# Performance work log

Hardware: AMD Instinct MI355X
Metric: run time of the kernel (lower is better)

## Reference

```python
import jax, jax.numpy as jnp
import numpy as np

N_HEAD = 16
LN_EPS = 1e-5     # torch LayerNorm default
ATTN_EPS = 1e-6   # fast-transformers CausalLinearAttention eps


def layer_norm(x, g, b):
    mu = x.mean(-1, keepdims=True)
    var = ((x - mu) ** 2).mean(-1, keepdims=True)
    return (x - mu) * jax.lax.rsqrt(var + LN_EPS) * g + b


def favor(x, omega):
    # Favor/Performer softmax-kernel features.
    # x: [B,S,H,dh], omega: [dh, m/2] -> phi: [B,S,H,m] with m = 2*(dh//2) = dh
    dh = x.shape[-1]
    m = 2 * omega.shape[-1]
    xs = x * (dh ** -0.25)  # x * sqrt(softmax_temp), softmax_temp = 1/sqrt(dh)
    u = jnp.einsum('bshd,dm->bshm', xs, omega)
    h = 0.5 * jnp.sum(xs * xs, axis=-1, keepdims=True)  # ||x||^2 / 2
    return jnp.concatenate([jnp.exp(u - h), jnp.exp(-u - h)], axis=-1) * (m ** -0.5)


def causal_linear_attention(q, k, v):
    # q,k: [B,S,H,M] feature-mapped; v: [B,S,H,Dv]
    # out[i] = (phiQ_i @ sum_{j<=i} phiK_j v_j^T) / (phiQ_i . sum_{j<=i} phiK_j)
    B, S, H, M = q.shape
    Dv = v.shape[-1]
    qT = jnp.moveaxis(q, 1, 0)  # [S,B,H,M]
    kT = jnp.moveaxis(k, 1, 0)
    vT = jnp.moveaxis(v, 1, 0)  # [S,B,H,Dv]
    S0 = jnp.zeros((B, H, M, Dv), q.dtype)
    z0 = jnp.zeros((B, H, M), q.dtype)

    def step(carry, qkv):
        Sst, zst = carry
        qi, ki, vi = qkv
        Sst = Sst + ki[..., :, None] * vi[..., None, :]  # [B,H,M,Dv]
        zst = zst + ki                                   # [B,H,M]
        num = jnp.einsum('bhm,bhmd->bhd', qi, Sst)
        den = jnp.einsum('bhm,bhm->bh', qi, zst) + ATTN_EPS
        return (Sst, zst), num / den[..., None]

    _, out = jax.lax.scan(step, (S0, z0), (qT, kT, vT))
    return jnp.moveaxis(out, 0, 1)  # [B,S,H,Dv]


def forward(x, Wq, bq, Wk, bk, Wv, bv, Wo, bo, omega,
            ln1_g, ln1_b, ln2_g, ln2_b, W1, bf1, W2, bf2):
    L = Wq.shape[0]
    B, S, D = x.shape
    dh = D // N_HEAD
    out = x
    for l in range(L):  # fixed small layer count
        q = (out @ Wq[l] + bq[l]).reshape(B, S, N_HEAD, dh)
        k = (out @ Wk[l] + bk[l]).reshape(B, S, N_HEAD, dh)
        v = (out @ Wv[l] + bv[l]).reshape(B, S, N_HEAD, dh)
        Qf = favor(q, omega[l])
        Kf = favor(k, omega[l])
        a = causal_linear_attention(Qf, Kf, v).reshape(B, S, D)
        a = a @ Wo[l] + bo[l]
        h = layer_norm(out + a, ln1_g[l], ln1_b[l])          # norm1 (post-norm)
        y = jax.nn.relu(h @ W1[l] + bf1[l]) @ W2[l] + bf2[l]  # FFN
        out = layer_norm(h + y, ln2_g[l], ln2_b[l])          # norm2
    return out


def setup_inputs() -> dict:
    key = jax.random.key(0)
    L, B, S, D, DFF = 3, 2, 1024, 1024, 4096
    dh = D // N_HEAD
    ks = jax.random.split(key, 8)
    g = lambda k, shape: jax.random.normal(k, shape, jnp.float32) * 0.02
    return {
        'x': jax.random.normal(ks[0], (B, S, D), jnp.float32),
        'Wq': g(ks[1], (L, D, D)), 'bq': jnp.zeros((L, D), jnp.float32),
        'Wk': g(ks[2], (L, D, D)), 'bk': jnp.zeros((L, D), jnp.float32),
        'Wv': g(ks[3], (L, D, D)), 'bv': jnp.zeros((L, D), jnp.float32),
        'Wo': g(ks[4], (L, D, D)), 'bo': jnp.zeros((L, D), jnp.float32),
        'omega': jax.random.normal(ks[5], (L, dh, dh // 2), jnp.float32),
        'ln1_g': jnp.ones((L, D), jnp.float32), 'ln1_b': jnp.zeros((L, D), jnp.float32),
        'ln2_g': jnp.ones((L, D), jnp.float32), 'ln2_b': jnp.zeros((L, D), jnp.float32),
        'W1': g(ks[6], (L, D, DFF)), 'bf1': jnp.zeros((L, DFF), jnp.float32),
        'W2': g(ks[7], (L, DFF, D)), 'bf2': jnp.zeros((L, D), jnp.float32),
    }


def reference(x, Wq, bq, Wk, bk, Wv, bv, Wo, bo, omega,
              ln1_g, ln1_b, ln2_g, ln2_b, W1, bf1, W2, bf2):
    return forward(x, Wq, bq, Wk, bk, Wv, bv, Wo, bo, omega,
                   ln1_g, ln1_b, ln2_g, ln2_b, W1, bf1, W2, bf2)
```

## Files before the change

kernel.cpp:

```cpp
#include <hip/hip_runtime.h>

typedef unsigned int u32;
typedef unsigned short u16;
typedef unsigned long long u64;

#define LN_EPS 1e-5f
#define ATTN_EPS 1e-6f

typedef __bf16 bf16x8 __attribute__((ext_vector_type(8)));
typedef short shortx8 __attribute__((ext_vector_type(8)));
typedef float fx4 __attribute__((ext_vector_type(4)));
typedef float fx16 __attribute__((ext_vector_type(16)));

__device__ __forceinline__ u16 f2bf(float f){
  union{float f; u32 u;} x; x.f = f;
  u32 r = 0x7fffu + ((x.u>>16)&1u);
  return (u16)((x.u + r)>>16);
}
__device__ __forceinline__ float bf2f(u16 u){
  union{u32 u; float f;} x; x.u = ((u32)u)<<16; return x.f;
}
__device__ __forceinline__ bf16x8 ldfrag(const u16* p){
  return __builtin_bit_cast(bf16x8, *(const shortx8*)p);
}

__device__ __forceinline__ void async16(const void* g, void* l){
  typedef const __attribute__((address_space(1))) void gas_t;
  typedef __attribute__((address_space(3))) void las_t;
  __builtin_amdgcn_global_load_lds((gas_t*)(u64)g, (las_t*)(u32)(u64)l, 16, 0, 0);
}

__global__ void detect_kernel(const u16* __restrict__ ln1g, int* __restrict__ flag){
  if (threadIdx.x == 0 && blockIdx.x == 0)
    *flag = (ln1g[0] == 0x3F80u) ? 1 : 0;
}

__global__ __launch_bounds__(256) void cvt_small(
    const void* p0, const void* p1, const void* p2, const void* p3,
    const void* p4, const void* p5, const void* p6, const void* p7,
    const void* p8, const void* p9, const void* p10,
    float* __restrict__ out, const int* __restrict__ flagp)
{
  int i = blockIdx.x*256 + threadIdx.x;
  if (i >= 46080) return;
  const void* src; int off;
  if      (i < 3072)  { src=p0;  off=i; }
  else if (i < 6144)  { src=p1;  off=i-3072; }
  else if (i < 9216)  { src=p2;  off=i-6144; }
  else if (i < 12288) { src=p3;  off=i-9216; }
  else if (i < 18432) { src=p4;  off=i-12288; }
  else if (i < 21504) { src=p5;  off=i-18432; }
  else if (i < 24576) { src=p6;  off=i-21504; }
  else if (i < 27648) { src=p7;  off=i-24576; }
  else if (i < 30720) { src=p8;  off=i-27648; }
  else if (i < 43008) { src=p9;  off=i-30720; }
  else                { src=p10; off=i-43008; }
  float v;
  if (*flagp){ union{u32 u; float f;} x; x.u = ((u32)((const u16*)src)[off])<<16; v = x.f; }
  else v = ((const float*)src)[off];
  out[i] = v;
}

__global__ __launch_bounds__(256) void cvt_x(const void* __restrict__ in, float* __restrict__ out,
                                             u16* __restrict__ outbf, int n, const int* __restrict__ flagp){
  int i = blockIdx.x*256 + threadIdx.x;
  if (i >= n) return;
  float v;
  if (*flagp){ union{u32 u; float f;} x; x.u = ((u32)((const u16*)in)[i])<<16; v = x.f; }
  else v = ((const float*)in)[i];
  out[i] = v;
  outbf[i] = f2bf(v);
}

__global__ __launch_bounds__(256) void transpose_cvtL(
    const void* __restrict__ W, u16* __restrict__ Wt,
    int K, int N, size_t zsrc, size_t zdst, const int* __restrict__ flagp)
{
  __shared__ float s[32][33];
  const size_t eoff = (size_t)blockIdx.z * zsrc;
  Wt += (size_t)blockIdx.z * zdst;
  const int bx = blockIdx.x, by = blockIdx.y;
  const int tid = threadIdx.x;
  const int c = tid & 31, r = tid >> 5;
  const int isbf = *flagp;
#pragma unroll
  for (int i = 0; i < 4; ++i){
    int k = by*32 + r + i*8, n = bx*32 + c;
    size_t idx = eoff + (size_t)k*N + n;
    float v;
    if (isbf){ union{u32 u; float f;} x; x.u = ((u32)((const u16*)W)[idx])<<16; v = x.f; }
    else v = ((const float*)W)[idx];
    s[r + i*8][c] = v;
  }
  __syncthreads();
#pragma unroll
  for (int i = 0; i < 4; ++i){
    int n = bx*32 + r + i*8, k = by*32 + c;
    Wt[(size_t)n*K + k] = f2bf(s[c][r + i*8]);
  }
}

__global__ __launch_bounds__(256) void transpose_cvtQ(
    const void* __restrict__ W0, const void* __restrict__ W1,
    const void* __restrict__ W2, const void* __restrict__ W3,
    u16* __restrict__ Wt, const int* __restrict__ flagp)
{
  __shared__ float s[32][33];
  const int z = blockIdx.z, l = z >> 2, m = z & 3;
  const void* W = (m==0)?W0:((m==1)?W1:((m==2)?W2:W3));
  const size_t eoff = (size_t)l * 1048576;
  Wt += (size_t)z * 1048576;
  const int bx = blockIdx.x, by = blockIdx.y;
  const int tid = threadIdx.x;
  const int c = tid & 31, r = tid >> 5;
  const int isbf = *flagp;
#pragma unroll
  for (int i = 0; i < 4; ++i){
    int k = by*32 + r + i*8, n = bx*32 + c;
    size_t idx = eoff + (size_t)k*1024 + n;
    float v;
    if (isbf){ union{u32 u; float f;} x; x.u = ((u32)((const u16*)W)[idx])<<16; v = x.f; }
    else v = ((const float*)W)[idx];
    s[r + i*8][c] = v;
  }
  __syncthreads();
#pragma unroll
  for (int i = 0; i < 4; ++i){
    int n = bx*32 + r + i*8, k = by*32 + c;
    Wt[(size_t)n*1024 + k] = f2bf(s[c][r + i*8]);
  }
}

__global__ __launch_bounds__(256, 2) void mfma_gemm(
    const u16* __restrict__ A, const u16* __restrict__ W,
    const float* __restrict__ bias,
    float* __restrict__ C, u16* __restrict__ Cbf,
    int N, int Kst, int kstep_z, int klen,
    size_t wz, size_t cz, int bz, int bias_all, int relu)
{
  __shared__ u16 As[2][128*64];
  __shared__ u16 Bs[2][128*64];
  const int z = blockIdx.z;
  W    += (size_t)z * wz;
  bias += (size_t)z * bz;
  if (C) C += (size_t)z * cz;
  const int kbeg = z * kstep_z;
  const int tid = threadIdx.x;
  const int lane = tid & 63, wid = tid >> 6;

  int bx = blockIdx.x, by = blockIdx.y;
  {
    const int gx = gridDim.x, gy = gridDim.y;
    if (((gx & 3) == 0) && ((gy & 1) == 0)) {
      const int cw = gx >> 2, ch = gy >> 1;
      if (((cw & (cw-1)) == 0) && ((ch & (ch-1)) == 0)) {
        const int o = by*gx + bx;
        const int xcd = o & 7, k = o >> 3;
        const int lgw = 31 - __clz(cw);
        bx = (xcd & 3)*cw + (k & (cw-1));
        by = (xcd >> 2)*ch + (k >> lgw);
      }
    }
  }
  const int row0 = by * 128, col0 = bx * 128;

  const int sR = tid >> 3;
  const int sC = ((tid & 7) ^ (sR & 7)) << 3;
  const u16* gA = A + (size_t)(row0 + sR)*Kst + kbeg + sC;
  const u16* gB = W + (size_t)(col0 + sR)*Kst + kbeg + sC;
  const int lb = tid*8;

  const int iters = klen >> 6;
#pragma unroll
  for (int i = 0; i < 4; ++i){
    async16(gA + (size_t)(32*i)*Kst, &As[0][i*2048 + lb]);
    async16(gB + (size_t)(32*i)*Kst, &Bs[0][i*2048 + lb]);
  }
  __builtin_amdgcn_s_waitcnt(0x0F70);
  __builtin_amdgcn_s_barrier();

  const int l31 = lane & 31, hi = lane >> 5;
  const int wr = (wid >> 1) * 64, wc = (wid & 1) * 64;
  fx16 acc[2][2] = {};

  for (int t = 0; t < iters; ++t){
    const int cur = t & 1;
    if (t + 1 < iters){
      const int ko = (t + 1) << 6;
#pragma unroll
      for (int i = 0; i < 4; ++i){
        async16(gA + (size_t)(32*i)*Kst + ko, &As[cur^1][i*2048 + lb]);
        async16(gB + (size_t)(32*i)*Kst + ko, &Bs[cur^1][i*2048 + lb]);
      }
    }
    bf16x8 af0[4], af1[4], bg0[4], bg1[4];
#pragma unroll
    for (int kh = 0; kh < 4; ++kh){
      const int sl = (((2*kh + hi) ^ (l31 & 7))) << 3;
      af0[kh] = ldfrag(&As[cur][(wr      + l31)*64 + sl]);
      af1[kh] = ldfrag(&As[cur][(wr + 32 + l31)*64 + sl]);
      bg0[kh] = ldfrag(&Bs[cur][(wc      + l31)*64 + sl]);
      bg1[kh] = ldfrag(&Bs[cur][(wc + 32 + l31)*64 + sl]);
    }
    __builtin_amdgcn_s_setprio(1);
#pragma unroll
    for (int kh = 0; kh < 4; ++kh){
      acc[0][0] = __builtin_amdgcn_mfma_f32_32x32x16_bf16(af0[kh], bg0[kh], acc[0][0], 0,0,0);
      acc[0][1] = __builtin_amdgcn_mfma_f32_32x32x16_bf16(af0[kh], bg1[kh], acc[0][1], 0,0,0);
      acc[1][0] = __builtin_amdgcn_mfma_f32_32x32x16_bf16(af1[kh], bg0[kh], acc[1][0], 0,0,0);
      acc[1][1] = __builtin_amdgcn_mfma_f32_32x32x16_bf16(af1[kh], bg1[kh], acc[1][1], 0,0,0);
    }
    __builtin_amdgcn_s_setprio(0);
    __builtin_amdgcn_s_waitcnt(0x0F70);
    __builtin_amdgcn_s_barrier();
  }

  const int rbase = 4*hi;
#pragma unroll
  for (int nt = 0; nt < 2; ++nt){
    const int col = col0 + wc + nt*32 + l31;
    const float bv = (bias_all || z == 0) ? bias[col] : 0.f;
#pragma unroll
    for (int mt = 0; mt < 2; ++mt){
#pragma unroll
      for (int r = 0; r < 16; ++r){
        const int row = row0 + wr + mt*32 + rbase + (r & 3) + 8*(r >> 2);
        float v = acc[mt][nt][r] + bv;
        if (relu) v = fmaxf(v, 0.f);
        if (C)   C[(size_t)row*N + col] = v;
        if (Cbf) Cbf[(size_t)row*N + col] = f2bf(v);
      }
    }
  }
}

__global__ __launch_bounds__(256) void favor_kernel(
    float* __restrict__ Q, float* __restrict__ Kp, const float* __restrict__ omega,
    u16* __restrict__ Qb, u16* __restrict__ Kb)
{
  __shared__ float sh[4][64];
  __shared__ float sho[64][32];
  int tid = threadIdx.x;
  for (int i = tid; i < 2048; i += 256)
    sho[i>>5][i&31] = omega[i];
  int wv = tid >> 6, lane = tid & 63;
  int th = blockIdx.x*4 + wv;
  size_t base = (size_t)(th >> 4) * 1024 + (size_t)(th & 15) * 64;
  int jm = lane & 31;
  float sgn = (lane < 32) ? 1.f : -1.f;
  for (int w = 0; w < 2; ++w){
    float* p = w ? Kp : Q;
    float xs = p[base + lane] * 0.35355339059327373f;
    __syncthreads();
    sh[wv][lane] = xs;
    __syncthreads();
    float u = 0.f, hh = 0.f;
#pragma unroll
    for (int d = 0; d < 64; ++d){
      float xv = sh[wv][d];
      u  = fmaf(xv, sho[d][jm], u);
      hh = fmaf(xv, xv, hh);
    }
    float phi = expf(sgn*u - 0.5f*hh) * 0.125f;
    if (w) p[base + lane] = phi;
    (w ? Kb : Qb)[base + lane] = f2bf(phi);
  }
}

__global__ __launch_bounds__(256) void chunk_kv(
    const float* __restrict__ Kf, const float* __restrict__ V,
    float* __restrict__ KV, float* __restrict__ Ksum)
{
  __shared__ float Ks[64][64];
  __shared__ float Vs[64][64];
  int blk = blockIdx.x;
  int c = blk & 15, h = (blk >> 4) & 15, b = blk >> 8;
  int tid = threadIdx.x;
  for (int i = tid; i < 1024; i += 256){
    int j = i >> 4, m4 = (i & 15) << 2;
    size_t src = ((size_t)(b*1024 + c*64 + j)*16 + h)*64 + m4;
    *(float4*)&Ks[j][m4] = *(const float4*)&Kf[src];
    *(float4*)&Vs[j][m4] = *(const float4*)&V[src];
  }
  __syncthreads();
  int m = tid & 63, dg = tid >> 6;
  float acc[16] = {0.f};
  for (int j = 0; j < 64; ++j){
    float kv = Ks[j][m];
#pragma unroll
    for (int di = 0; di < 16; ++di)
      acc[di] = fmaf(Vs[j][dg*16+di], kv, acc[di]);
  }
  size_t outb = (size_t)blk * 4096;
#pragma unroll
  for (int di = 0; di < 16; ++di)
    KV[outb + (size_t)(dg*16+di)*64 + m] = acc[di];
  if (tid < 64){
    float s = 0.f;
    for (int j = 0; j < 64; ++j) s += Ks[j][tid];
    Ksum[(size_t)blk*64 + tid] = s;
  }
}

__global__ __launch_bounds__(256) void chunk_scan(float* __restrict__ KV, float* __restrict__ Ksum)
{
  int blk = blockIdx.x;
  int bh = blk >> 4, ec = blk & 15;
  int e = ec*256 + threadIdx.x;
  size_t base = (size_t)bh * 65536 + e;
  float run = 0.f;
  for (int c = 0; c < 16; ++c){
    size_t idx = base + (size_t)c*4096;
    float t = KV[idx]; KV[idx] = run; run += t;
  }
  if (ec == 0 && threadIdx.x < 64){
    size_t kb = (size_t)bh * 1024 + threadIdx.x;
    float rz = 0.f;
    for (int c = 0; c < 16; ++c){
      size_t idx = kb + c*64;
      float t = Ksum[idx]; Ksum[idx] = rz; rz += t;
    }
  }
}

__global__ __launch_bounds__(256) void attn_kernel(
    const u16* __restrict__ Qbf, const u16* __restrict__ Kbf,
    const float* __restrict__ V, const float* __restrict__ KVt,
    const float* __restrict__ Ksum, u16* __restrict__ Outbf)
{
  __shared__ u16 Qs[64][72];
  __shared__ u16 Ks[64][72];
  __shared__ u16 Ss[64][72];
  __shared__ u16 Vt[64][72];
  __shared__ u16 Pt[64][72];
  __shared__ float Vrow[64][68];
  __shared__ float densum[64];

  const int blk = blockIdx.x;
  const int c = blk & 15, h = (blk >> 4) & 15, b = blk >> 8;
  const int tid = threadIdx.x;
  const int lane = tid & 63, w = tid >> 6;
  const int quad = lane >> 4, l16 = lane & 15;
  const int t0 = b*1024 + c*64;

  {
    const int r = tid >> 2, q4 = (tid & 3) << 4;
    size_t g = (size_t)(t0 + r)*1024 + h*64 + q4;
    *(uint4*)&Qs[r][q4]   = *(const uint4*)(Qbf + g);
    *(uint4*)&Qs[r][q4+8] = *(const uint4*)(Qbf + g + 8);
    *(uint4*)&Ks[r][q4]   = *(const uint4*)(Kbf + g);
    *(uint4*)&Ks[r][q4+8] = *(const uint4*)(Kbf + g + 8);
    const float* vg = V + g;
    *(float4*)&Vrow[r][q4+0]  = *(const float4*)(vg+0);
    *(float4*)&Vrow[r][q4+4]  = *(const float4*)(vg+4);
    *(float4*)&Vrow[r][q4+8]  = *(const float4*)(vg+8);
    *(float4*)&Vrow[r][q4+12] = *(const float4*)(vg+12);
    const float* pg = KVt + (size_t)blk*4096 + r*64 + q4;
    u16 tmp[16];
#pragma unroll
    for (int j = 0; j < 16; ++j) tmp[j] = f2bf(pg[j]);
    *(uint4*)&Pt[r][q4]   = *(uint4*)&tmp[0];
    *(uint4*)&Pt[r][q4+8] = *(uint4*)&tmp[8];
  }
  __syncthreads();
  {
    const int d = tid >> 2, j16 = (tid & 3) << 4;
    u16 tmp[16];
#pragma unroll
    for (int j = 0; j < 16; ++j) tmp[j] = f2bf(Vrow[j16+j][d]);
    *(uint4*)&Vt[d][j16]   = *(uint4*)&tmp[0];
    *(uint4*)&Vt[d][j16+8] = *(uint4*)&tmp[8];
  }

  const int iw0 = w*16;
  bf16x8 aq0 = ldfrag(&Qs[iw0+l16][quad*8]);
  bf16x8 aq1 = ldfrag(&Qs[iw0+l16][32+quad*8]);
  fx4 sacc[4];
#pragma unroll
  for (int u = 0; u < 4; ++u){
    sacc[u] = (fx4){0.f,0.f,0.f,0.f};
    bf16x8 b0 = ldfrag(&Ks[u*16+l16][quad*8]);
    bf16x8 b1 = ldfrag(&Ks[u*16+l16][32+quad*8]);
    sacc[u] = __builtin_amdgcn_mfma_f32_16x16x32_bf16(aq0, b0, sacc[u], 0, 0, 0);
    sacc[u] = __builtin_amdgcn_mfma_f32_16x16x32_bf16(aq1, b1, sacc[u], 0, 0, 0);
  }
  float rs[4] = {0.f,0.f,0.f,0.f};
#pragma unroll
  for (int u = 0; u < 4; ++u){
    const int jl = u*16 + l16;
#pragma unroll
    for (int r = 0; r < 4; ++r){
      const int il = iw0 + quad*4 + r;
      float v = (jl <= il) ? sacc[u][r] : 0.f;
      rs[r] += v;
      Ss[il][jl] = f2bf(v);
    }
  }
#pragma unroll
  for (int off = 1; off < 16; off <<= 1){
#pragma unroll
    for (int r = 0; r < 4; ++r) rs[r] += __shfl_xor(rs[r], off);
  }
  if (l16 == 0){
#pragma unroll
    for (int r = 0; r < 4; ++r) densum[iw0 + quad*4 + r] = rs[r];
  }
  __syncthreads();

  {
    const int row = iw0 + l16;
    const float* zp = Ksum + (size_t)blk*64;
    float dp = 0.f;
#pragma unroll
    for (int m = 0; m < 16; ++m){
      const int mm = quad*16 + m;
      dp = fmaf(bf2f(Qs[row][mm]), zp[mm], dp);
    }
    dp += __shfl_xor(dp, 16);
    dp += __shfl_xor(dp, 32);
    if (quad == 0) densum[row] = densum[row] + dp + ATTN_EPS;
  }
  __syncthreads();

  bf16x8 as0 = ldfrag(&Ss[iw0+l16][quad*8]);
  bf16x8 as1 = ldfrag(&Ss[iw0+l16][32+quad*8]);
  fx4 oacc[4];
#pragma unroll
  for (int u = 0; u < 4; ++u){
    const int d0 = u*16;
    oacc[u] = (fx4){0.f,0.f,0.f,0.f};
    oacc[u] = __builtin_amdgcn_mfma_f32_16x16x32_bf16(as0, ldfrag(&Vt[d0+l16][quad*8]),    oacc[u], 0,0,0);
    oacc[u] = __builtin_amdgcn_mfma_f32_16x16x32_bf16(as1, ldfrag(&Vt[d0+l16][32+quad*8]), oacc[u], 0,0,0);
    oacc[u] = __builtin_amdgcn_mfma_f32_16x16x32_bf16(aq0, ldfrag(&Pt[d0+l16][quad*8]),    oacc[u], 0,0,0);
    oacc[u] = __builtin_amdgcn_mfma_f32_16x16x32_bf16(aq1, ldfrag(&Pt[d0+l16][32+quad*8]), oacc[u], 0,0,0);
  }
#pragma unroll
  for (int u = 0; u < 4; ++u){
    const int d = u*16 + l16;
#pragma unroll
    for (int r = 0; r < 4; ++r){
      const int il = iw0 + quad*4 + r;
      const float o = oacc[u][r] / densum[il];
      Outbf[(size_t)(t0 + il)*1024 + h*64 + d] = f2bf(o);
    }
  }
}

__global__ __launch_bounds__(256) void resid_ln(
    const float* __restrict__ X, const float* __restrict__ Y0, const float* __restrict__ Y1,
    const float* __restrict__ Y2, const float* __restrict__ Y3,
    const float* __restrict__ g, const float* __restrict__ b,
    float* __restrict__ Dst, u16* __restrict__ DstBf,
    void* __restrict__ OutPtr, const int* __restrict__ flagp)
{
  __shared__ float rs[4], rss[4];
  int row = blockIdx.x, tid = threadIdx.x;
  int lane = tid & 63, wv = tid >> 6;
  size_t base = (size_t)row * 1024;
  int c = tid << 2;
  float4 xv = *(const float4*)&X[base + c];
  float4 y0 = *(const float4*)&Y0[base + c];
  float4 y1 = *(const float4*)&Y1[base + c];
  float v0 = xv.x+y0.x+y1.x, v1 = xv.y+y0.y+y1.y, v2 = xv.z+y0.z+y1.z, v3 = xv.w+y0.w+y1.w;
  if (Y2){
    float4 y2 = *(const float4*)&Y2[base + c];
    float4 y3 = *(const float4*)&Y3[base + c];
    v0 += y2.x + y3.x; v1 += y2.y + y3.y; v2 += y2.z + y3.z; v3 += y2.w + y3.w;
  }
  float s = v0+v1+v2+v3;
  float ss = v0*v0+v1*v1+v2*v2+v3*v3;
  for (int off = 32; off; off >>= 1){
    s  += __shfl_down(s, off);
    ss += __shfl_down(ss, off);
  }
  if (lane == 0){ rs[wv] = s; rss[wv] = ss; }
  __syncthreads();
  float S  = rs[0]+rs[1]+rs[2]+rs[3];
  float SS = rss[0]+rss[1]+rss[2]+rss[3];
  float mu = S * (1.f/1024.f);
  float var = SS * (1.f/1024.f) - mu*mu;
  float rinv = rsqrtf(var + LN_EPS);
  float4 gv = *(const float4*)(g + c);
  float4 bb = *(const float4*)(b + c);
  float o0 = (v0-mu)*rinv*gv.x + bb.x;
  float o1 = (v1-mu)*rinv*gv.y + bb.y;
  float o2 = (v2-mu)*rinv*gv.z + bb.z;
  float o3 = (v3-mu)*rinv*gv.w + bb.w;
  *(float4*)&Dst[base + c] = make_float4(o0,o1,o2,o3);
  uint2 ob;
  ob.x = (u32)f2bf(o0) | ((u32)f2bf(o1) << 16);
  ob.y = (u32)f2bf(o2) | ((u32)f2bf(o3) << 16);
  *(uint2*)(DstBf + base + c) = ob;
  if (OutPtr){
    if (*flagp){
      *(uint2*)((u16*)OutPtr + base + c) = ob;
    } else {
      *(float4*)((float*)OutPtr + base + c) = make_float4(o0,o1,o2,o3);
    }
  }
}

extern "C" void kernel_launch(void* const* d_in, const int* in_sizes, int n_in,
                              void* d_out, int out_size, void* d_ws, size_t ws_size,
                              hipStream_t stream)
{
  (void)in_sizes; (void)n_in; (void)out_size; (void)ws_size;

  float* ws   = (float*)d_ws;
  float* R    = ws;
  float* P0   = R  + 2097152;
  float* P1   = P0 + 2097152;
  float* P2   = P1 + 2097152;
  float* P3   = P2 + 2097152;
  float* KVb  = P3 + 2097152;
  float* Ks   = KVb + 2097152;
  float* smallP = Ks + 32768;
  float* pend = smallP + 46080;
  int* flag = (int*)pend;
  u16* abf  = (u16*)(pend + 4);
  u16* hbf  = abf  + 2097152;
  u16* t1bf = hbf  + 2097152;
  u16* fbf  = t1bf + 2097152;
  u16* qpbf = fbf  + 8388608;
  u16* kpbf = qpbf + 2097152;
  u16* WtQ  = kpbf + 2097152;
  u16* WtF1 = WtQ  + 12582912;
  u16* WtF2 = WtF1 + 12582912;

  float* bqF  = smallP + 0;
  float* boF  = smallP + 9216;
  float* omF  = smallP + 12288;
  float* l1gF = smallP + 18432;
  float* l1bF = smallP + 21504;
  float* l2gF = smallP + 24576;
  float* l2bF = smallP + 27648;
  float* bf1F = smallP + 30720;
  float* bf2F = smallP + 43008;

  detect_kernel<<<1, 64, 0, stream>>>((const u16*)d_in[10], flag);
  cvt_small<<<180, 256, 0, stream>>>(d_in[2], d_in[4], d_in[6], d_in[8], d_in[9],
                                     d_in[10], d_in[11], d_in[12], d_in[13],
                                     d_in[15], d_in[17], smallP, flag);
  cvt_x<<<8192, 256, 0, stream>>>(d_in[0], R, abf, 2097152, flag);

  transpose_cvtQ<<<dim3(32, 32, 12), 256, 0, stream>>>(d_in[1], d_in[3], d_in[5], d_in[7],
                                                       WtQ, flag);
  transpose_cvtL<<<dim3(128, 32, 3), 256, 0, stream>>>(d_in[14], WtF1, 1024, 4096,
                                                       4194304, 4194304, flag);
  transpose_cvtL<<<dim3(32, 128, 3), 256, 0, stream>>>(d_in[16], WtF2, 4096, 1024,
                                                       4194304, 4194304, flag);

  dim3 gQKV(8, 16, 3);
  dim3 gO(8, 16, 2);
  dim3 gF1(32, 16, 1);
  dim3 gF2(8, 16, 4);

  for (int l = 0; l < 3; ++l){
    const size_t wQ = (size_t)l * 4194304;

    mfma_gemm<<<gQKV, 256, 0, stream>>>(abf, WtQ + wQ, bqF + l*1024, P0, (u16*)nullptr,
                                        1024, 1024, 0, 1024,
                                        1048576, 2097152, 3072, 1, 0);
    favor_kernel<<<8192, 256, 0, stream>>>(P0, P1, omF + l*2048, qpbf, kpbf);
    chunk_kv<<<512, 256, 0, stream>>>(P1, P2, KVb, Ks);
    chunk_scan<<<512, 256, 0, stream>>>(KVb, Ks);
    attn_kernel<<<512, 256, 0, stream>>>(qpbf, kpbf, P2, KVb, Ks, t1bf);

    mfma_gemm<<<gO, 256, 0, stream>>>(t1bf, WtQ + wQ + 3145728, boF + l*1024, P0, (u16*)nullptr,
                                      1024, 1024, 512, 512,
                                      0, 2097152, 0, 0, 0);
    resid_ln<<<2048, 256, 0, stream>>>(R, P0, P1, nullptr, nullptr,
                                       l1gF + l*1024, l1bF + l*1024,
                                       KVb, hbf, nullptr, flag);

    mfma_gemm<<<gF1, 256, 0, stream>>>(hbf, WtF1 + wQ, bf1F + l*4096, (float*)nullptr, fbf,
                                       4096, 1024, 0, 1024,
                                       0, 0, 0, 1, 1);

    mfma_gemm<<<gF2, 256, 0, stream>>>(fbf, WtF2 + wQ, bf2F + l*1024, P0, (u16*)nullptr,
                                       1024, 4096, 1024, 1024,
                                       0, 2097152, 0, 0, 0);

    resid_ln<<<2048, 256, 0, stream>>>(KVb, P0, P1, P2, P3,
                                       l2gF + l*1024, l2bF + l*1024,
                                       R, abf, (l == 2) ? d_out : nullptr, flag);
  }
}
```

Baseline: 727.5 us.

## Switch GEMM to 256x128 tiles with 8 waves and triple-buffered split staging

The bf16 MFMA GEMM now uses 512-thread blocks computing 256x128 output tiles, with three LDS buffers and a prefetch distance of two k-steps. Each k-step's global-to-LDS copy is split into two halves interleaved with the two halves of the MFMA work. The goal is to hide global-load latency and reuse the B tile across more rows. In exchange the grids halve in the M dimension: the QKV and O-projection launches drop to 192 and 128 blocks, which can leave CUs idle. The 144KB of LDS limits occupancy to one block per CU.

```diff
diff --git a/kernel.cpp b/kernel.cpp
--- a/kernel.cpp
+++ b/kernel.cpp
@@ -131,15 +131,15 @@
   }
 }
 
-__global__ __launch_bounds__(256, 2) void mfma_gemm(
+__global__ __launch_bounds__(512, 2) void mfma_gemm8(
     const u16* __restrict__ A, const u16* __restrict__ W,
     const float* __restrict__ bias,
     float* __restrict__ C, u16* __restrict__ Cbf,
     int N, int Kst, int kstep_z, int klen,
     size_t wz, size_t cz, int bz, int bias_all, int relu)
 {
-  __shared__ u16 As[2][128*64];
-  __shared__ u16 Bs[2][128*64];
+  __shared__ u16 As[3][256*64];
+  __shared__ u16 Bs[3][128*64];
   const int z = blockIdx.z;
   W    += (size_t)z * wz;
   bias += (size_t)z * bz;
@@ -147,6 +147,7 @@
   const int kbeg = z * kstep_z;
   const int tid = threadIdx.x;
   const int lane = tid & 63, wid = tid >> 6;
+  const size_t KstS = (size_t)Kst;
 
   int bx = blockIdx.x, by = blockIdx.y;
   {
@@ -162,76 +163,108 @@
       }
     }
   }
-  const int row0 = by * 128, col0 = bx * 128;
+  const int row0 = by * 256, col0 = bx * 128;
 
   const int sR = tid >> 3;
   const int sC = ((tid & 7) ^ (sR & 7)) << 3;
-  const u16* gA = A + (size_t)(row0 + sR)*Kst + kbeg + sC;
-  const u16* gB = W + (size_t)(col0 + sR)*Kst + kbeg + sC;
-  const int lb = tid*8;
-
-  const int iters = klen >> 6;
-#pragma unroll
-  for (int i = 0; i < 4; ++i){
-    async16(gA + (size_t)(32*i)*Kst, &As[0][i*2048 + lb]);
-    async16(gB + (size_t)(32*i)*Kst, &Bs[0][i*2048 + lb]);
+  const u16* gAr = A + (size_t)(row0 + sR)*KstS + kbeg + sC;
+  const u16* gBr = W + (size_t)(col0 + sR)*KstS + kbeg + sC;
+
+#define STAGE_H0(b, ks) { const size_t ko = (size_t)(ks) << 6; \
+    async16(gAr + ko,                &As[b][tid*8]); \
+    async16(gAr + 64*KstS + ko,      &As[b][4096 + tid*8]); \
+    async16(gBr + ko,                &Bs[b][tid*8]); }
+#define STAGE_H1(b, ks) { const size_t ko = (size_t)(ks) << 6; \
+    async16(gAr + 128*KstS + ko,     &As[b][8192 + tid*8]); \
+    async16(gAr + 192*KstS + ko,     &As[b][12288 + tid*8]); \
+    async16(gBr + 64*KstS + ko,      &Bs[b][4096 + tid*8]); }
+
+  const int nt = klen >> 6;
+  STAGE_H0(0, 0) STAGE_H1(0, 0)
+  STAGE_H0(1, 1) STAGE_H1(1, 1)
+  __builtin_amdgcn_s_waitcnt(0x0F76);
+  __builtin_amdgcn_s_barrier();
+
+  const int l31 = lane & 31, hi = lane >> 5;
+  const int wr = (wid >> 1) * 64;
+  const int wc = (wid & 1) * 64;
+  fx16 acc[2][2] = {};
+
+  for (int t = 0; t < nt; ++t){
+    const int buf = t % 3;
+    const int nx   = (t + 2 < nt) ? (t + 2) : (nt - 1);
+    const int nbuf = (t + 2) % 3;
+
+    bf16x8 a0[2][2], b0[2][2];
+#pragma unroll
+    for (int kk = 0; kk < 2; ++kk){
+      const int sl = ((2*kk + hi) ^ (l31 & 7)) << 3;
+#pragma unroll
+      for (int mt = 0; mt < 2; ++mt)
+        a0[mt][kk] = ldfrag(&As[buf][(wr + mt*32 + l31)*64 + sl]);
+#pragma unroll
+      for (int ntc = 0; ntc < 2; ++ntc)
+        b0[ntc][kk] = ldfrag(&Bs[buf][(wc + ntc*32 + l31)*64 + sl]);
+    }
+    STAGE_H0(nbuf, nx)
+    __builtin_amdgcn_s_barrier();
+    __builtin_amdgcn_s_setprio(1);
+#pragma unroll
+    for (int kk = 0; kk < 2; ++kk)
+#pragma unroll
+      for (int mt = 0; mt < 2; ++mt)
+#pragma unroll
+        for (int ntc = 0; ntc < 2; ++ntc)
+          acc[mt][ntc] = __builtin_amdgcn_mfma_f32_32x32x16_bf16(a0[mt][kk], b0[ntc][kk], acc[mt][ntc], 0,0,0);
+    __builtin_amdgcn_s_setprio(0);
+    __builtin_amdgcn_s_barrier();
+
+    bf16x8 a1[2][2], b1[2][2];
+#pragma unroll
+    for (int kk = 0; kk < 2; ++kk){
+      const int sl = ((2*(kk+2) + hi) ^ (l31 & 7)) << 3;
+#pragma unroll
+      for (int mt = 0; mt < 2; ++mt)
+        a1[mt][kk] = ldfrag(&As[buf][(wr + mt*32 + l31)*64 + sl]);
+#pragma unroll
+      for (int ntc = 0; ntc < 2; ++ntc)
+        b1[ntc][kk] = ldfrag(&Bs[buf][(wc + ntc*32 + l31)*64 + sl]);
+    }
+    STAGE_H1(nbuf, nx)
+    __builtin_amdgcn_s_waitcnt(0x0F76);
+    __builtin_amdgcn_s_barrier();
+    __builtin_amdgcn_s_setprio(1);
+#pragma unroll
+    for (int kk = 0; kk < 2; ++kk)
+#pragma unroll
+      for (int mt = 0; mt < 2; ++mt)
+#pragma unroll
+        for (int ntc = 0; ntc < 2; ++ntc)
+          acc[mt][ntc] = __builtin_amdgcn_mfma_f32_32x32x16_bf16(a1[mt][kk], b1[ntc][kk], acc[mt][ntc], 0,0,0);
+    __builtin_amdgcn_s_setprio(0);
+    __builtin_amdgcn_s_barrier();
   }
   __builtin_amdgcn_s_waitcnt(0x0F70);
-  __builtin_amdgcn_s_barrier();
-
-  const int l31 = lane & 31, hi = lane >> 5;
-  const int wr = (wid >> 1) * 64, wc = (wid & 1) * 64;
-  fx16 acc[2][2] = {};
-
-  for (int t = 0; t < iters; ++t){
-    const int cur = t & 1;
-    if (t + 1 < iters){
-      const int ko = (t + 1) << 6;
-#pragma unroll
-      for (int i = 0; i < 4; ++i){
-        async16(gA + (size_t)(32*i)*Kst + ko, &As[cur^1][i*2048 + lb]);
-        async16(gB + (size_t)(32*i)*Kst + ko, &Bs[cur^1][i*2048 + lb]);
-      }
-    }
-    bf16x8 af0[4], af1[4], bg0[4], bg1[4];
-#pragma unroll
-    for (int kh = 0; kh < 4; ++kh){
-      const int sl = (((2*kh + hi) ^ (l31 & 7))) << 3;
-      af0[kh] = ldfrag(&As[cur][(wr      + l31)*64 + sl]);
-      af1[kh] = ldfrag(&As[cur][(wr + 32 + l31)*64 + sl]);
-      bg0[kh] = ldfrag(&Bs[cur][(wc      + l31)*64 + sl]);
-      bg1[kh] = ldfrag(&Bs[cur][(wc + 32 + l31)*64 + sl]);
-    }
-    __builtin_amdgcn_s_setprio(1);
-#pragma unroll
-    for (int kh = 0; kh < 4; ++kh){
-      acc[0][0] = __builtin_amdgcn_mfma_f32_32x32x16_bf16(af0[kh], bg0[kh], acc[0][0], 0,0,0);
-      acc[0][1] = __builtin_amdgcn_mfma_f32_32x32x16_bf16(af0[kh], bg1[kh], acc[0][1], 0,0,0);
-      acc[1][0] = __builtin_amdgcn_mfma_f32_32x32x16_bf16(af1[kh], bg0[kh], acc[1][0], 0,0,0);
-      acc[1][1] = __builtin_amdgcn_mfma_f32_32x32x16_bf16(af1[kh], bg1[kh], acc[1][1], 0,0,0);
-    }
-    __builtin_amdgcn_s_setprio(0);
-    __builtin_amdgcn_s_waitcnt(0x0F70);
-    __builtin_amdgcn_s_barrier();
-  }
 
   const int rbase = 4*hi;
 #pragma unroll
-  for (int nt = 0; nt < 2; ++nt){
-    const int col = col0 + wc + nt*32 + l31;
+  for (int ntc = 0; ntc < 2; ++ntc){
+    const int col = col0 + wc + ntc*32 + l31;
     const float bv = (bias_all || z == 0) ? bias[col] : 0.f;
 #pragma unroll
     for (int mt = 0; mt < 2; ++mt){
 #pragma unroll
       for (int r = 0; r < 16; ++r){
         const int row = row0 + wr + mt*32 + rbase + (r & 3) + 8*(r >> 2);
-        float v = acc[mt][nt][r] + bv;
+        float v = acc[mt][ntc][r] + bv;
         if (relu) v = fmaxf(v, 0.f);
         if (C)   C[(size_t)row*N + col] = v;
         if (Cbf) Cbf[(size_t)row*N + col] = f2bf(v);
       }
     }
   }
+#undef STAGE_H0
+#undef STAGE_H1
 }
 
 __global__ __launch_bounds__(256) void favor_kernel(
@@ -550,36 +583,36 @@
   transpose_cvtL<<<dim3(32, 128, 3), 256, 0, stream>>>(d_in[16], WtF2, 4096, 1024,
                                                        4194304, 4194304, flag);
 
-  dim3 gQKV(8, 16, 3);
-  dim3 gO(8, 16, 2);
-  dim3 gF1(32, 16, 1);
-  dim3 gF2(8, 16, 4);
+  dim3 gQKV(8, 8, 3);
+  dim3 gO(8, 8, 2);
+  dim3 gF1(32, 8, 1);
+  dim3 gF2(8, 8, 4);
 
   for (int l = 0; l < 3; ++l){
     const size_t wQ = (size_t)l * 4194304;
 
-    mfma_gemm<<<gQKV, 256, 0, stream>>>(abf, WtQ + wQ, bqF + l*1024, P0, (u16*)nullptr,
-                                        1024, 1024, 0, 1024,
-                                        1048576, 2097152, 3072, 1, 0);
+    mfma_gemm8<<<gQKV, 512, 0, stream>>>(abf, WtQ + wQ, bqF + l*1024, P0, (u16*)nullptr,
+                                         1024, 1024, 0, 1024,
+                                         1048576, 2097152, 3072, 1, 0);
     favor_kernel<<<8192, 256, 0, stream>>>(P0, P1, omF + l*2048, qpbf, kpbf);
     chunk_kv<<<512, 256, 0, stream>>>(P1, P2, KVb, Ks);
     chunk_scan<<<512, 256, 0, stream>>>(KVb, Ks);
     attn_kernel<<<512, 256, 0, stream>>>(qpbf, kpbf, P2, KVb, Ks, t1bf);
 
-    mfma_gemm<<<gO, 256, 0, stream>>>(t1bf, WtQ + wQ + 3145728, boF + l*1024, P0, (u16*)nullptr,
-                                      1024, 1024, 512, 512,
-                                      0, 2097152, 0, 0, 0);
+    mfma_gemm8<<<gO, 512, 0, stream>>>(t1bf, WtQ + wQ + 3145728, boF + l*1024, P0, (u16*)nullptr,
+                                       1024, 1024, 512, 512,
+                                       0, 2097152, 0, 0, 0);
     resid_ln<<<2048, 256, 0, stream>>>(R, P0, P1, nullptr, nullptr,
                                        l1gF + l*1024, l1bF + l*1024,
                                        KVb, hbf, nullptr, flag);
 
-    mfma_gemm<<<gF1, 256, 0, stream>>>(hbf, WtF1 + wQ, bf1F + l*4096, (float*)nullptr, fbf,
-                                       4096, 1024, 0, 1024,
-                                       0, 0, 0, 1, 1);
-
-    mfma_gemm<<<gF2, 256, 0, stream>>>(fbf, WtF2 + wQ, bf2F + l*1024, P0, (u16*)nullptr,
-                                       1024, 4096, 1024, 1024,
-                                       0, 2097152, 0, 0, 0);
+    mfma_gemm8<<<gF1, 512, 0, stream>>>(hbf, WtF1 + wQ, bf1F + l*4096, (float*)nullptr, fbf,
+                                        4096, 1024, 0, 1024,
+                                        0, 0, 0, 1, 1);
+
+    mfma_gemm8<<<gF2, 512, 0, stream>>>(fbf, WtF2 + wQ, bf2F + l*1024, P0, (u16*)nullptr,
+                                        1024, 4096, 1024, 1024,
+                                        0, 2097152, 0, 0, 0);
 
     resid_ln<<<2048, 256, 0, stream>>>(KVb, P0, P1, P2, P3,
                                        l2gF + l*1024, l2bF + l*1024,
```

Measured after the change: 721.3 us. About the same (-0.8%).
